# Kernel optimization log

Hardware: AMD Instinct MI355X
Metric: run time of the kernel (lower is better)

## Reference

```python
import math
import jax, jax.numpy as jnp
import numpy as np

N_GAUSS = 1_000_000
EPS = 1e-8


def setup_inputs() -> dict:
    key = jax.random.key(0)
    k1, k2, k3 = jax.random.split(key, 3)
    init_extent = 50.0
    means = (jax.random.uniform(k1, (N_GAUSS, 3), dtype=jnp.float32) - 0.5) * 2.0 * init_extent
    log_scales = jnp.full((N_GAUSS, 3), math.log(0.05), dtype=jnp.float32)
    quats = jax.random.normal(k2, (N_GAUSS, 4), dtype=jnp.float32)
    sh_coeffs = jax.random.normal(k3, (N_GAUSS, 16, 3), dtype=jnp.float32) * 0.01
    opa_logit = math.log(0.1 / 0.9)  # inverse_sigmoid(init_opacity=0.1)
    opacity_camera = jnp.full((N_GAUSS, 1), opa_logit, dtype=jnp.float32)
    opacity_lidar = jnp.full((N_GAUSS, 1), opa_logit, dtype=jnp.float32)
    camera_to_world = jnp.eye(4, dtype=jnp.float32)
    lidar_to_world = jnp.eye(4, dtype=jnp.float32)
    intrinsics = jnp.array([[1000.0, 0.0, 800.0], [0.0, 1000.0, 450.0], [0.0, 0.0, 1.0]], dtype=jnp.float32)
    return dict(means=means, log_scales=log_scales, quats=quats, sh_coeffs=sh_coeffs,
                opacity_camera=opacity_camera, opacity_lidar=opacity_lidar,
                camera_to_world=camera_to_world, intrinsics=intrinsics,
                lidar_to_world=lidar_to_world,
                rgb_width=1600, rgb_height=900, lidar_width=1024, lidar_height=128,
                fov_min_deg=-25, fov_max_deg=3, near_plane=1, far_plane=100)


def _bilinear_scatter(u, v, w, vals, H, W, wrap_u):
    """Scatter vals [N,C] with weights w [N] at continuous pixel coords (u,v)
    using bilinear splatting. Returns [H, W, C+1] (weighted vals, weight sum)."""
    u0 = jnp.floor(u)
    v0 = jnp.floor(v)
    fu = u - u0
    fv = v - v0
    u0i = u0.astype(jnp.int32)
    v0i = v0.astype(jnp.int32)
    acc = jnp.zeros((H * W, vals.shape[-1] + 1), dtype=vals.dtype)
    corners = ((0, 0, (1.0 - fu) * (1.0 - fv)), (1, 0, fu * (1.0 - fv)),
               (0, 1, (1.0 - fu) * fv), (1, 1, fu * fv))
    for du, dv, cw in corners:
        ui = u0i + du
        vi = v0i + dv
        if wrap_u:
            ui = jnp.mod(ui, W)
            ok_u = jnp.ones_like(ui, dtype=bool)
        else:
            ok_u = (ui >= 0) & (ui < W)
        ok = ok_u & (vi >= 0) & (vi < H)
        ww = w * cw * ok.astype(w.dtype)
        idx = jnp.clip(vi, 0, H - 1) * W + jnp.clip(ui, 0, W - 1)
        payload = jnp.concatenate([vals * ww[:, None], ww[:, None]], axis=-1)
        acc = acc.at[idx].add(payload)
    return acc.reshape(H, W, -1)


def reference(means, log_scales, quats, sh_coeffs, opacity_camera, opacity_lidar,
              camera_to_world, intrinsics, lidar_to_world,
              rgb_width, rgb_height, lidar_width, lidar_height,
              fov_min_deg, fov_max_deg, near_plane, far_plane):
    H, W = int(rgb_height), int(rgb_width)
    HL, WL = int(lidar_height), int(lidar_width)
    near = float(near_plane)
    far = float(far_plane)

    # ---- camera (point-splat proxy of gsplat rasterization) ----
    w2c = jnp.linalg.inv(camera_to_world)
    pts_c = means @ w2c[:3, :3].T + w2c[:3, 3]  # [N,3] camera frame
    x, y, z = pts_c[:, 0], pts_c[:, 1], pts_c[:, 2]
    valid_c = (z > near) & (z < far)
    zs = jnp.where(valid_c, z, 1.0)
    u = intrinsics[0, 0] * x / zs + intrinsics[0, 2]
    v = intrinsics[1, 1] * y / zs + intrinsics[1, 2]
    opa_c = jax.nn.sigmoid(jnp.clip(opacity_camera[:, 0], -20.0, 20.0))
    colors = jax.nn.sigmoid(sh_coeffs[:, 0, :])  # DC band, as in render_rgb
    wc = opa_c * valid_c.astype(opa_c.dtype)
    vals_c = jnp.concatenate([colors, z[:, None]], axis=-1)  # [N,4] (rgb, depth)
    acc = _bilinear_scatter(u, v, wc, vals_c, H, W, wrap_u=False)
    wsum = acc[..., 4]
    alpha = jnp.clip(wsum, 0.0, 1.0)
    rgb = acc[..., :3] / (wsum[..., None] + EPS) * alpha[..., None]  # black background
    depth = acc[..., 3] / (wsum + EPS)

    # ---- LiDAR (custom spherical bilinear range-image splat, mean aggregation) ----
    w2l = jnp.linalg.inv(lidar_to_world)
    pts_l = means @ w2l[:3, :3].T + w2l[:3, 3]
    r = jnp.linalg.norm(pts_l, axis=-1)
    az = jnp.arctan2(pts_l[:, 1], pts_l[:, 0])
    el = jnp.arcsin(pts_l[:, 2] / jnp.maximum(r, 1e-6))
    fmin = math.radians(float(fov_min_deg))
    fmax = math.radians(float(fov_max_deg))
    uL = (az / (2.0 * jnp.pi) + 0.5) * WL          # azimuth wraps around
    vL = (fmax - el) / (fmax - fmin) * (HL - 1)    # elevation row
    valid_l = (r > near) & (r < far) & (el >= fmin) & (el <= fmax)
    opa_l = jax.nn.sigmoid(jnp.clip(opacity_lidar[:, 0], -20.0, 20.0))
    wl = opa_l * valid_l.astype(opa_l.dtype)
    acc_l = _bilinear_scatter(uL, vL, wl, r[:, None], HL, WL, wrap_u=True)
    lw = acc_l[..., 1]
    lidar_depth = acc_l[..., 0] / (lw + EPS)  # 'mean' depth aggregation
    lidar_alpha = jnp.clip(lw, 0.0, 1.0)

    return (rgb, depth, alpha, lidar_depth, lidar_alpha)
```

## Files before the change

### kernel.cpp

```cpp
#include <hip/hip_runtime.h>
#include <math.h>

#define EPSV 1e-8f
#define PI_D 3.14159265358979323846

__device__ __forceinline__ void invert4x4_reg(const float* __restrict__ m,
                                              float* __restrict__ out) {
    double a00=m[0], a01=m[1], a02=m[2], a03=m[3];
    double a10=m[4], a11=m[5], a12=m[6], a13=m[7];
    double a20=m[8], a21=m[9], a22=m[10],a23=m[11];
    double a30=m[12],a31=m[13],a32=m[14],a33=m[15];

    double b00 = a00*a11 - a01*a10;
    double b01 = a00*a12 - a02*a10;
    double b02 = a00*a13 - a03*a10;
    double b03 = a01*a12 - a02*a11;
    double b04 = a01*a13 - a03*a11;
    double b05 = a02*a13 - a03*a12;
    double b06 = a20*a31 - a21*a30;
    double b07 = a20*a32 - a22*a30;
    double b08 = a20*a33 - a23*a30;
    double b09 = a21*a32 - a22*a31;
    double b10 = a21*a33 - a23*a31;
    double b11 = a22*a33 - a23*a32;

    double det = b00*b11 - b01*b10 + b02*b09 + b03*b08 - b04*b07 + b05*b06;
    double inv = 1.0 / det;

    out[0]  = (float)(( a11*b11 - a12*b10 + a13*b09) * inv);
    out[1]  = (float)((-a01*b11 + a02*b10 - a03*b09) * inv);
    out[2]  = (float)(( a31*b05 - a32*b04 + a33*b03) * inv);
    out[3]  = (float)((-a21*b05 + a22*b04 - a23*b03) * inv);
    out[4]  = (float)((-a10*b11 + a12*b08 - a13*b07) * inv);
    out[5]  = (float)(( a00*b11 - a02*b08 + a03*b07) * inv);
    out[6]  = (float)((-a30*b05 + a32*b02 - a33*b01) * inv);
    out[7]  = (float)(( a20*b05 - a22*b02 + a23*b01) * inv);
    out[8]  = (float)(( a10*b10 - a11*b08 + a13*b06) * inv);
    out[9]  = (float)((-a00*b10 + a01*b08 - a03*b06) * inv);
    out[10] = (float)(( a30*b04 - a31*b02 + a33*b00) * inv);
    out[11] = (float)((-a20*b04 + a21*b02 - a23*b00) * inv);
    out[12] = (float)((-a10*b09 + a11*b07 - a12*b06) * inv);
    out[13] = (float)(( a00*b09 - a01*b07 + a02*b06) * inv);
    out[14] = (float)((-a30*b03 + a31*b01 - a32*b00) * inv);
    out[15] = (float)(( a20*b03 - a21*b01 + a22*b00) * inv);
}

__global__ void prep_kernel(const float* __restrict__ c2w,
                            const float* __restrict__ l2w,
                            float* __restrict__ ws) {
    if (blockIdx.x == 0 && threadIdx.x == 0) {
        invert4x4_reg(c2w, ws);
        invert4x4_reg(l2w, ws + 16);
    }
}

__device__ __forceinline__ float sigmoid_clipped(float x) {
    #pragma clang fp contract(off)
    x = fminf(fmaxf(x, -20.0f), 20.0f);
    return 1.0f / (1.0f + expf(-x));
}

__global__ __launch_bounds__(256) void scatter_kernel(
    const float* __restrict__ means,
    const float* __restrict__ sh,
    const float* __restrict__ opa_c,
    const float* __restrict__ opa_l,
    const float* __restrict__ intr,
    const float* __restrict__ ws,
    const int* __restrict__ p_W, const int* __restrict__ p_H,
    const int* __restrict__ p_WL, const int* __restrict__ p_HL,
    const int* __restrict__ p_fmin, const int* __restrict__ p_fmax,
    const int* __restrict__ p_near, const int* __restrict__ p_far,
    float* __restrict__ out, int N)
{
    #pragma clang fp contract(off)
    const int T = (N + 3) >> 2;
    const int t = blockIdx.x * blockDim.x + threadIdx.x;
    if (t >= T) return;

    const int W = *p_W, H = *p_H, WL = *p_WL, HL = *p_HL;
    const float nearp = (float)(*p_near);
    const float farp  = (float)(*p_far);
    const double dfmin = (double)(*p_fmin) * PI_D / 180.0;
    const double dfmax = (double)(*p_fmax) * PI_D / 180.0;
    const float ffmin  = (float)dfmin;
    const float ffmax  = (float)dfmax;
    const float denomL = (float)(dfmax - dfmin);
    const float twopi  = (float)(2.0 * PI_D);

    const long long HW = (long long)W * H;
    const long long LHW = (long long)WL * HL;
    const long long depthOff = 3 * HW;
    const long long alphaOff = 4 * HW;
    const long long ldOff    = 5 * HW;
    const long long laOff    = 5 * HW + LHW;

    const float fx = intr[0], cx = intr[2], fy = intr[4], cy = intr[5];
    const float* w2c = ws;
    const float* w2l = ws + 16;

    float mx[4], my[4], mz[4], oc[4], ol[4];
    int   gi[4];
    bool  gv[4];
    #pragma unroll
    for (int k = 0; k < 4; k++) {
        int i = t + k * T;
        gv[k] = (i < N);
        int ii = gv[k] ? i : 0;
        gi[k] = ii;
        mx[k] = means[3 * ii + 0];
        my[k] = means[3 * ii + 1];
        mz[k] = means[3 * ii + 2];
        oc[k] = opa_c[ii];
        ol[k] = opa_l[ii];
    }

    #pragma unroll
    for (int k = 0; k < 4; k++) {
        if (!gv[k]) continue;
        const float px = mx[k], py = my[k], pz = mz[k];

        {
            float x = w2c[0] * px + w2c[1] * py + w2c[2]  * pz + w2c[3];
            float y = w2c[4] * px + w2c[5] * py + w2c[6]  * pz + w2c[7];
            float z = w2c[8] * px + w2c[9] * py + w2c[10] * pz + w2c[11];
            if (z > nearp && z < farp) {
                float u = fx * x / z + cx;
                float v = fy * y / z + cy;
                float wc = sigmoid_clipped(oc[k]);
                const float* shp = sh + 48LL * gi[k];
                float c0 = 1.0f / (1.0f + expf(-shp[0]));
                float c1 = 1.0f / (1.0f + expf(-shp[1]));
                float c2 = 1.0f / (1.0f + expf(-shp[2]));

                float u0f = floorf(u), v0f = floorf(v);
                float fu = u - u0f, fv = v - v0f;
                int u0 = (int)u0f, v0 = (int)v0f;
                #pragma unroll
                for (int c = 0; c < 4; c++) {
                    int du = c & 1, dv = c >> 1;
                    int ui = u0 + du, vi = v0 + dv;
                    if (ui >= 0 && ui < W && vi >= 0 && vi < H) {
                        float cw = (du ? fu : 1.0f - fu) * (dv ? fv : 1.0f - fv);
                        float ww = wc * cw;
                        long long idx = (long long)vi * W + ui;
                        atomicAdd(&out[idx * 3 + 0], c0 * ww);
                        atomicAdd(&out[idx * 3 + 1], c1 * ww);
                        atomicAdd(&out[idx * 3 + 2], c2 * ww);
                        atomicAdd(&out[depthOff + idx], z * ww);
                        atomicAdd(&out[alphaOff + idx], ww);
                    }
                }
            }
        }

        {
            float x = w2l[0] * px + w2l[1] * py + w2l[2]  * pz + w2l[3];
            float y = w2l[4] * px + w2l[5] * py + w2l[6]  * pz + w2l[7];
            float z = w2l[8] * px + w2l[9] * py + w2l[10] * pz + w2l[11];
            float rr = ((x * x) + (y * y)) + (z * z);
            float r = sqrtf(rr);
            float q  = z / fmaxf(r, 1e-6f);
            float el = (float)asin((double)q);
            if (r > nearp && r < farp && el >= ffmin && el <= ffmax) {
                float az = (float)atan2((double)y, (double)x);
                float uL = (az / twopi + 0.5f) * (float)WL;
                float vL = (ffmax - el) / denomL * (float)(HL - 1);
                float wl = sigmoid_clipped(ol[k]);

                float u0f = floorf(uL), v0f = floorf(vL);
                float fu = uL - u0f, fv = vL - v0f;
                int u0 = (int)u0f, v0 = (int)v0f;
                #pragma unroll
                for (int c = 0; c < 4; c++) {
                    int du = c & 1, dv = c >> 1;
                    int ui = u0 + du, vi = v0 + dv;
                    ui %= WL; if (ui < 0) ui += WL;
                    if (vi >= 0 && vi < HL) {
                        float cw = (du ? fu : 1.0f - fu) * (dv ? fv : 1.0f - fv);
                        float ww = wl * cw;
                        long long idx = (long long)vi * WL + ui;
                        atomicAdd(&out[ldOff + idx], r * ww);
                        atomicAdd(&out[laOff + idx], ww);
                    }
                }
            }
        }
    }
}

__global__ __launch_bounds__(256) void finalize_kernel(
    float* __restrict__ out,
    const int* __restrict__ p_W, const int* __restrict__ p_H,
    const int* __restrict__ p_WL, const int* __restrict__ p_HL)
{
    const int W = *p_W, H = *p_H, WL = *p_WL, HL = *p_HL;
    const long long HW = (long long)W * H;
    const long long LHW = (long long)WL * HL;
    const long long depthOff = 3 * HW;
    const long long alphaOff = 4 * HW;
    const long long ldOff    = 5 * HW;
    const long long laOff    = 5 * HW + LHW;

    long long i = (long long)blockIdx.x * blockDim.x + threadIdx.x;
    if (i < HW) {
        float wsum = out[alphaOff + i];
        float a = fminf(fmaxf(wsum, 0.0f), 1.0f);
        float inv = 1.0f / (wsum + EPSV);
        float s = inv * a;
        out[3 * i + 0] *= s;
        out[3 * i + 1] *= s;
        out[3 * i + 2] *= s;
        out[depthOff + i] *= inv;
        out[alphaOff + i] = a;
    }
    if (i < LHW) {
        float wsum = out[laOff + i];
        out[ldOff + i] *= 1.0f / (wsum + EPSV);
        out[laOff + i] = fminf(fmaxf(wsum, 0.0f), 1.0f);
    }
}

extern "C" void kernel_launch(void* const* d_in, const int* in_sizes, int n_in,
                              void* d_out, int out_size, void* d_ws, size_t ws_size,
                              hipStream_t stream) {
    const float* means  = (const float*)d_in[0];
    const float* sh     = (const float*)d_in[3];
    const float* opa_c  = (const float*)d_in[4];
    const float* opa_l  = (const float*)d_in[5];
    const float* c2w    = (const float*)d_in[6];
    const float* intr   = (const float*)d_in[7];
    const float* l2w    = (const float*)d_in[8];
    const int* p_W    = (const int*)d_in[9];
    const int* p_H    = (const int*)d_in[10];
    const int* p_WL   = (const int*)d_in[11];
    const int* p_HL   = (const int*)d_in[12];
    const int* p_fmin = (const int*)d_in[13];
    const int* p_fmax = (const int*)d_in[14];
    const int* p_near = (const int*)d_in[15];
    const int* p_far  = (const int*)d_in[16];

    const int N = in_sizes[0] / 3;
    float* out = (float*)d_out;
    float* ws  = (float*)d_ws;

    hipMemsetAsync(d_out, 0, (size_t)out_size * sizeof(float), stream);

    prep_kernel<<<1, 64, 0, stream>>>(c2w, l2w, ws);

    const int T = (N + 3) / 4;
    scatter_kernel<<<(T + 255) / 256, 256, 0, stream>>>(
        means, sh, opa_c, opa_l, intr, ws,
        p_W, p_H, p_WL, p_HL, p_fmin, p_fmax, p_near, p_far,
        out, N);

    const long long HW = 1600LL * 900LL;
    finalize_kernel<<<(int)((HW + 255) / 256), 256, 0, stream>>>(
        out, p_W, p_H, p_WL, p_HL);
}
```

Measured before the change: 423.9 us.

## Accumulate splats into interleaved 8-float per-pixel records in workspace

```diff
diff --git a/kernel.cpp b/kernel.cpp
--- a/kernel.cpp
+++ b/kernel.cpp
@@ -3,6 +3,9 @@
 
 #define EPSV 1e-8f
 #define PI_D 3.14159265358979323846
+
+#define HW_C  (1600LL * 900LL)
+#define LHW_C (1024LL * 128LL)
 
 __device__ __forceinline__ void invert4x4_reg(const float* __restrict__ m,
                                               float* __restrict__ out) {
@@ -60,6 +63,141 @@
     return 1.0f / (1.0f + expf(-x));
 }
 
+__global__ __launch_bounds__(256) void scatter_ws_kernel(
+    const float* __restrict__ means,
+    const float* __restrict__ sh,
+    const float* __restrict__ opa_c,
+    const float* __restrict__ opa_l,
+    const float* __restrict__ intr,
+    const float* __restrict__ ws,
+    const int* __restrict__ p_W, const int* __restrict__ p_H,
+    const int* __restrict__ p_WL, const int* __restrict__ p_HL,
+    const int* __restrict__ p_fmin, const int* __restrict__ p_fmax,
+    const int* __restrict__ p_near, const int* __restrict__ p_far,
+    float* __restrict__ acc, int N)
+{
+    #pragma clang fp contract(off)
+    const int i = blockIdx.x * blockDim.x + threadIdx.x;
+    if (i >= N) return;
+
+    const int W = *p_W, H = *p_H, WL = *p_WL, HL = *p_HL;
+    const float nearp = (float)(*p_near);
+    const float farp  = (float)(*p_far);
+    const double dfmin = (double)(*p_fmin) * PI_D / 180.0;
+    const double dfmax = (double)(*p_fmax) * PI_D / 180.0;
+    const float ffmin  = (float)dfmin;
+    const float ffmax  = (float)dfmax;
+    const float denomL = (float)(dfmax - dfmin);
+    const float twopi  = (float)(2.0 * PI_D);
+
+    const long long HW = (long long)W * H;
+    float* __restrict__ lacc = acc + 8 * HW;
+
+    const float px = means[3 * i + 0];
+    const float py = means[3 * i + 1];
+    const float pz = means[3 * i + 2];
+    const float* w2c = ws;
+    const float* w2l = ws + 16;
+
+    {
+        float x = w2c[0] * px + w2c[1] * py + w2c[2]  * pz + w2c[3];
+        float y = w2c[4] * px + w2c[5] * py + w2c[6]  * pz + w2c[7];
+        float z = w2c[8] * px + w2c[9] * py + w2c[10] * pz + w2c[11];
+        if (z > nearp && z < farp) {
+            float u = intr[0] * x / z + intr[2];
+            float v = intr[4] * y / z + intr[5];
+            float wc = sigmoid_clipped(opa_c[i]);
+            const float* shp = sh + 48LL * i;
+            float c0 = 1.0f / (1.0f + expf(-shp[0]));
+            float c1 = 1.0f / (1.0f + expf(-shp[1]));
+            float c2 = 1.0f / (1.0f + expf(-shp[2]));
+
+            float u0f = floorf(u), v0f = floorf(v);
+            float fu = u - u0f, fv = v - v0f;
+            int u0 = (int)u0f, v0 = (int)v0f;
+            #pragma unroll
+            for (int c = 0; c < 4; c++) {
+                int du = c & 1, dv = c >> 1;
+                int ui = u0 + du, vi = v0 + dv;
+                if (ui >= 0 && ui < W && vi >= 0 && vi < H) {
+                    float cw = (du ? fu : 1.0f - fu) * (dv ? fv : 1.0f - fv);
+                    float ww = wc * cw;
+                    float* rec = acc + 8LL * ((long long)vi * W + ui);
+                    atomicAdd(rec + 0, c0 * ww);
+                    atomicAdd(rec + 1, c1 * ww);
+                    atomicAdd(rec + 2, c2 * ww);
+                    atomicAdd(rec + 3, z * ww);
+                    atomicAdd(rec + 4, ww);
+                }
+            }
+        }
+    }
+
+    {
+        float x = w2l[0] * px + w2l[1] * py + w2l[2]  * pz + w2l[3];
+        float y = w2l[4] * px + w2l[5] * py + w2l[6]  * pz + w2l[7];
+        float z = w2l[8] * px + w2l[9] * py + w2l[10] * pz + w2l[11];
+        float rr = ((x * x) + (y * y)) + (z * z);
+        float r = sqrtf(rr);
+        float q  = z / fmaxf(r, 1e-6f);
+        float el = (float)asin((double)q);
+        if (r > nearp && r < farp && el >= ffmin && el <= ffmax) {
+            float az = (float)atan2((double)y, (double)x);
+            float uL = (az / twopi + 0.5f) * (float)WL;
+            float vL = (ffmax - el) / denomL * (float)(HL - 1);
+            float wl = sigmoid_clipped(opa_l[i]);
+
+            float u0f = floorf(uL), v0f = floorf(vL);
+            float fu = uL - u0f, fv = vL - v0f;
+            int u0 = (int)u0f, v0 = (int)v0f;
+            #pragma unroll
+            for (int c = 0; c < 4; c++) {
+                int du = c & 1, dv = c >> 1;
+                int ui = u0 + du, vi = v0 + dv;
+                ui %= WL; if (ui < 0) ui += WL;
+                if (vi >= 0 && vi < HL) {
+                    float cw = (du ? fu : 1.0f - fu) * (dv ? fv : 1.0f - fv);
+                    float ww = wl * cw;
+                    float* rec = lacc + 2LL * ((long long)vi * WL + ui);
+                    atomicAdd(rec + 0, r * ww);
+                    atomicAdd(rec + 1, ww);
+                }
+            }
+        }
+    }
+}
+
+__global__ __launch_bounds__(256) void finalize_ws_kernel(
+    const float* __restrict__ acc,
+    float* __restrict__ out,
+    const int* __restrict__ p_W, const int* __restrict__ p_H,
+    const int* __restrict__ p_WL, const int* __restrict__ p_HL)
+{
+    const int W = *p_W, H = *p_H, WL = *p_WL, HL = *p_HL;
+    const long long HW = (long long)W * H;
+    const long long LHW = (long long)WL * HL;
+    const float* __restrict__ lacc = acc + 8 * HW;
+
+    long long i = (long long)blockIdx.x * blockDim.x + threadIdx.x;
+    if (i < HW) {
+        const float* rec = acc + 8 * i;
+        float r0 = rec[0], r1 = rec[1], r2 = rec[2], zw = rec[3], wsum = rec[4];
+        float a = fminf(fmaxf(wsum, 0.0f), 1.0f);
+        float inv = 1.0f / (wsum + EPSV);
+        float s = inv * a;
+        out[3 * i + 0] = r0 * s;
+        out[3 * i + 1] = r1 * s;
+        out[3 * i + 2] = r2 * s;
+        out[3 * HW + i] = zw * inv;
+        out[4 * HW + i] = a;
+    }
+    if (i < LHW) {
+        float rw = lacc[2 * i], wsum = lacc[2 * i + 1];
+        out[5 * HW + i]       = rw * (1.0f / (wsum + EPSV));
+        out[5 * HW + LHW + i] = fminf(fmaxf(wsum, 0.0f), 1.0f);
+    }
+}
+
 __global__ __launch_bounds__(256) void scatter_kernel(
     const float* __restrict__ means,
     const float* __restrict__ sh,
@@ -74,9 +212,8 @@
     float* __restrict__ out, int N)
 {
     #pragma clang fp contract(off)
-    const int T = (N + 3) >> 2;
-    const int t = blockIdx.x * blockDim.x + threadIdx.x;
-    if (t >= T) return;
+    const int i = blockIdx.x * blockDim.x + threadIdx.x;
+    if (i >= N) return;
 
     const int W = *p_W, H = *p_H, WL = *p_WL, HL = *p_HL;
     const float nearp = (float)(*p_near);
@@ -95,94 +232,73 @@
     const long long ldOff    = 5 * HW;
     const long long laOff    = 5 * HW + LHW;
 
-    const float fx = intr[0], cx = intr[2], fy = intr[4], cy = intr[5];
+    const float px = means[3 * i + 0];
+    const float py = means[3 * i + 1];
+    const float pz = means[3 * i + 2];
     const float* w2c = ws;
     const float* w2l = ws + 16;
 
-    float mx[4], my[4], mz[4], oc[4], ol[4];
-    int   gi[4];
-    bool  gv[4];
-    #pragma unroll
-    for (int k = 0; k < 4; k++) {
-        int i = t + k * T;
-        gv[k] = (i < N);
-        int ii = gv[k] ? i : 0;
-        gi[k] = ii;
-        mx[k] = means[3 * ii + 0];
-        my[k] = means[3 * ii + 1];
-        mz[k] = means[3 * ii + 2];
-        oc[k] = opa_c[ii];
-        ol[k] = opa_l[ii];
-    }
-
-    #pragma unroll
-    for (int k = 0; k < 4; k++) {
-        if (!gv[k]) continue;
-        const float px = mx[k], py = my[k], pz = mz[k];
-
-        {
-            float x = w2c[0] * px + w2c[1] * py + w2c[2]  * pz + w2c[3];
-            float y = w2c[4] * px + w2c[5] * py + w2c[6]  * pz + w2c[7];
-            float z = w2c[8] * px + w2c[9] * py + w2c[10] * pz + w2c[11];
-            if (z > nearp && z < farp) {
-                float u = fx * x / z + cx;
-                float v = fy * y / z + cy;
-                float wc = sigmoid_clipped(oc[k]);
-                const float* shp = sh + 48LL * gi[k];
-                float c0 = 1.0f / (1.0f + expf(-shp[0]));
-                float c1 = 1.0f / (1.0f + expf(-shp[1]));
-                float c2 = 1.0f / (1.0f + expf(-shp[2]));
-
-                float u0f = floorf(u), v0f = floorf(v);
-                float fu = u - u0f, fv = v - v0f;
-                int u0 = (int)u0f, v0 = (int)v0f;
-                #pragma unroll
-                for (int c = 0; c < 4; c++) {
-                    int du = c & 1, dv = c >> 1;
-                    int ui = u0 + du, vi = v0 + dv;
-                    if (ui >= 0 && ui < W && vi >= 0 && vi < H) {
-                        float cw = (du ? fu : 1.0f - fu) * (dv ? fv : 1.0f - fv);
-                        float ww = wc * cw;
-                        long long idx = (long long)vi * W + ui;
-                        atomicAdd(&out[idx * 3 + 0], c0 * ww);
-                        atomicAdd(&out[idx * 3 + 1], c1 * ww);
-                        atomicAdd(&out[idx * 3 + 2], c2 * ww);
-                        atomicAdd(&out[depthOff + idx], z * ww);
-                        atomicAdd(&out[alphaOff + idx], ww);
-                    }
+    {
+        float x = w2c[0] * px + w2c[1] * py + w2c[2]  * pz + w2c[3];
+        float y = w2c[4] * px + w2c[5] * py + w2c[6]  * pz + w2c[7];
+        float z = w2c[8] * px + w2c[9] * py + w2c[10] * pz + w2c[11];
+        if (z > nearp && z < farp) {
+            float u = intr[0] * x / z + intr[2];
+            float v = intr[4] * y / z + intr[5];
+            float wc = sigmoid_clipped(opa_c[i]);
+            const float* shp = sh + 48LL * i;
+            float c0 = 1.0f / (1.0f + expf(-shp[0]));
+            float c1 = 1.0f / (1.0f + expf(-shp[1]));
+            float c2 = 1.0f / (1.0f + expf(-shp[2]));
+
+            float u0f = floorf(u), v0f = floorf(v);
+            float fu = u - u0f, fv = v - v0f;
+            int u0 = (int)u0f, v0 = (int)v0f;
+            #pragma unroll
+            for (int c = 0; c < 4; c++) {
+                int du = c & 1, dv = c >> 1;
+                int ui = u0 + du, vi = v0 + dv;
+                if (ui >= 0 && ui < W && vi >= 0 && vi < H) {
+                    float cw = (du ? fu : 1.0f - fu) * (dv ? fv : 1.0f - fv);
+                    float ww = wc * cw;
+                    long long idx = (long long)vi * W + ui;
+                    atomicAdd(&out[idx * 3 + 0], c0 * ww);
+                    atomicAdd(&out[idx * 3 + 1], c1 * ww);
+                    atomicAdd(&out[idx * 3 + 2], c2 * ww);
+                    atomicAdd(&out[depthOff + idx], z * ww);
+                    atomicAdd(&out[alphaOff + idx], ww);
                 }
             }
         }
-
-        {
-            float x = w2l[0] * px + w2l[1] * py + w2l[2]  * pz + w2l[3];
-            float y = w2l[4] * px + w2l[5] * py + w2l[6]  * pz + w2l[7];
-            float z = w2l[8] * px + w2l[9] * py + w2l[10] * pz + w2l[11];
-            float rr = ((x * x) + (y * y)) + (z * z);
-            float r = sqrtf(rr);
-            float q  = z / fmaxf(r, 1e-6f);
-            float el = (float)asin((double)q);
-            if (r > nearp && r < farp && el >= ffmin && el <= ffmax) {
-                float az = (float)atan2((double)y, (double)x);
-                float uL = (az / twopi + 0.5f) * (float)WL;
-                float vL = (ffmax - el) / denomL * (float)(HL - 1);
-                float wl = sigmoid_clipped(ol[k]);
-
-                float u0f = floorf(uL), v0f = floorf(vL);
-                float fu = uL - u0f, fv = vL - v0f;
-                int u0 = (int)u0f, v0 = (int)v0f;
-                #pragma unroll
-                for (int c = 0; c < 4; c++) {
-                    int du = c & 1, dv = c >> 1;
-                    int ui = u0 + du, vi = v0 + dv;
-                    ui %= WL; if (ui < 0) ui += WL;
-                    if (vi >= 0 && vi < HL) {
-                        float cw = (du ? fu : 1.0f - fu) * (dv ? fv : 1.0f - fv);
-                        float ww = wl * cw;
-                        long long idx = (long long)vi * WL + ui;
-                        atomicAdd(&out[ldOff + idx], r * ww);
-                        atomicAdd(&out[laOff + idx], ww);
-                    }
+    }
+    {
+        float x = w2l[0] * px + w2l[1] * py + w2l[2]  * pz + w2l[3];
+        float y = w2l[4] * px + w2l[5] * py + w2l[6]  * pz + w2l[7];
+        float z = w2l[8] * px + w2l[9] * py + w2l[10] * pz + w2l[11];
+        float rr = ((x * x) + (y * y)) + (z * z);
+        float r = sqrtf(rr);
+        float q  = z / fmaxf(r, 1e-6f);
+        float el = (float)asin((double)q);
+        if (r > nearp && r < farp && el >= ffmin && el <= ffmax) {
+            float az = (float)atan2((double)y, (double)x);
+            float uL = (az / twopi + 0.5f) * (float)WL;
+            float vL = (ffmax - el) / denomL * (float)(HL - 1);
+            float wl = sigmoid_clipped(opa_l[i]);
+
+            float u0f = floorf(uL), v0f = floorf(vL);
+            float fu = uL - u0f, fv = vL - v0f;
+            int u0 = (int)u0f, v0 = (int)v0f;
+            #pragma unroll
+            for (int c = 0; c < 4; c++) {
+                int du = c & 1, dv = c >> 1;
+                int ui = u0 + du, vi = v0 + dv;
+                ui %= WL; if (ui < 0) ui += WL;
+                if (vi >= 0 && vi < HL) {
+                    float cw = (du ? fu : 1.0f - fu) * (dv ? fv : 1.0f - fv);
+                    float ww = wl * cw;
+                    long long idx = (long long)vi * WL + ui;
+                    atomicAdd(&out[ldOff + idx], r * ww);
+                    atomicAdd(&out[laOff + idx], ww);
                 }
             }
         }
@@ -197,27 +313,23 @@
     const int W = *p_W, H = *p_H, WL = *p_WL, HL = *p_HL;
     const long long HW = (long long)W * H;
     const long long LHW = (long long)WL * HL;
-    const long long depthOff = 3 * HW;
-    const long long alphaOff = 4 * HW;
-    const long long ldOff    = 5 * HW;
-    const long long laOff    = 5 * HW + LHW;
 
     long long i = (long long)blockIdx.x * blockDim.x + threadIdx.x;
     if (i < HW) {
-        float wsum = out[alphaOff + i];
+        float wsum = out[4 * HW + i];
         float a = fminf(fmaxf(wsum, 0.0f), 1.0f);
         float inv = 1.0f / (wsum + EPSV);
         float s = inv * a;
         out[3 * i + 0] *= s;
         out[3 * i + 1] *= s;
         out[3 * i + 2] *= s;
-        out[depthOff + i] *= inv;
-        out[alphaOff + i] = a;
+        out[3 * HW + i] *= inv;
+        out[4 * HW + i] = a;
     }
     if (i < LHW) {
-        float wsum = out[laOff + i];
-        out[ldOff + i] *= 1.0f / (wsum + EPSV);
-        out[laOff + i] = fminf(fmaxf(wsum, 0.0f), 1.0f);
+        float wsum = out[5 * HW + LHW + i];
+        out[5 * HW + i] *= 1.0f / (wsum + EPSV);
+        out[5 * HW + LHW + i] = fminf(fmaxf(wsum, 0.0f), 1.0f);
     }
 }
 
@@ -244,17 +356,28 @@
     float* out = (float*)d_out;
     float* ws  = (float*)d_ws;
 
-    hipMemsetAsync(d_out, 0, (size_t)out_size * sizeof(float), stream);
+    const size_t accFloats = 8 * (size_t)HW_C + 2 * (size_t)LHW_C;
+    const size_t wsNeeded  = (32 + accFloats) * sizeof(float);
+    const bool fast = (ws_size >= wsNeeded);
 
     prep_kernel<<<1, 64, 0, stream>>>(c2w, l2w, ws);
 
-    const int T = (N + 3) / 4;
-    scatter_kernel<<<(T + 255) / 256, 256, 0, stream>>>(
-        means, sh, opa_c, opa_l, intr, ws,
-        p_W, p_H, p_WL, p_HL, p_fmin, p_fmax, p_near, p_far,
-        out, N);
-
-    const long long HW = 1600LL * 900LL;
-    finalize_kernel<<<(int)((HW + 255) / 256), 256, 0, stream>>>(
-        out, p_W, p_H, p_WL, p_HL);
-}
+    if (fast) {
+        float* acc = ws + 32;
+        hipMemsetAsync(acc, 0, accFloats * sizeof(float), stream);
+        scatter_ws_kernel<<<(N + 255) / 256, 256, 0, stream>>>(
+            means, sh, opa_c, opa_l, intr, ws,
+            p_W, p_H, p_WL, p_HL, p_fmin, p_fmax, p_near, p_far,
+            acc, N);
+        finalize_ws_kernel<<<(int)((HW_C + 255) / 256), 256, 0, stream>>>(
+            acc, out, p_W, p_H, p_WL, p_HL);
+    } else {
+        hipMemsetAsync(d_out, 0, (size_t)out_size * sizeof(float), stream);
+        scatter_kernel<<<(N + 255) / 256, 256, 0, stream>>>(
+            means, sh, opa_c, opa_l, intr, ws,
+            p_W, p_H, p_WL, p_HL, p_fmin, p_fmax, p_near, p_far,
+            out, N);
+        finalize_kernel<<<(int)((HW_C + 255) / 256), 256, 0, stream>>>(
+            out, p_W, p_H, p_WL, p_HL);
+    }
+}
```

After: 426.8 us. About the same (+0.7%).
